# Kernel tuning notes

Hardware: AMD Instinct MI355X
Metric: run time of the kernel (lower is better)

The kernel has to match this reference:

```python
import jax, jax.numpy as jnp
import numpy as np
import math

NUM_HEADS = 16
HEAD_DIM = 64
ROPE_BASE = 10000.0

def _rope_tables(T, dtype):
    # inv_freq: (D/2,), emb = cat([freqs, freqs]) -> (T, D)
    inv_freq = 1.0 / (ROPE_BASE ** (jnp.arange(0, HEAD_DIM, 2, dtype=jnp.float32) / HEAD_DIM))
    t = jnp.arange(T, dtype=jnp.float32)
    freqs = jnp.einsum('i,j->ij', t, inv_freq)          # (T, D/2)
    emb = jnp.concatenate([freqs, freqs], axis=-1)      # (T, D)
    return jnp.cos(emb).astype(dtype), jnp.sin(emb).astype(dtype)

def _rotate_half(x):
    # interleaved pair rotation: (x0,x1,x2,x3,...) -> (-x1,x0,-x3,x2,...)
    x1 = x[..., ::2]
    x2 = x[..., 1::2]
    return jnp.stack((-x2, x1), axis=-1).reshape(x.shape)

def setup_inputs() -> dict:
    key = jax.random.key(0)
    ks = jax.random.split(key, 9)
    B, T, C = 2, 2048, 1024
    s = 1.0 / math.sqrt(C)
    return {
        'x':  jax.random.normal(ks[0], (B, T, C), dtype=jnp.float32),
        'wq': jax.random.normal(ks[1], (C, C), dtype=jnp.float32) * s,
        'bq': jax.random.normal(ks[2], (C,), dtype=jnp.float32) * s,
        'wk': jax.random.normal(ks[3], (C, C), dtype=jnp.float32) * s,
        'bk': jax.random.normal(ks[4], (C,), dtype=jnp.float32) * s,
        'wv': jax.random.normal(ks[5], (C, C), dtype=jnp.float32) * s,
        'bv': jax.random.normal(ks[6], (C,), dtype=jnp.float32) * s,
        'wo': jax.random.normal(ks[7], (C, C), dtype=jnp.float32) * s,
        'bo': jax.random.normal(ks[8], (C,), dtype=jnp.float32) * s,
    }

def reference(x, wq, bq, wk, bk, wv, bv, wo, bo):
    B, T, C = x.shape
    H, D = NUM_HEADS, HEAD_DIM

    def heads(t):  # (B,T,C) -> (B,H,T,D)
        return t.reshape(B, T, H, D).transpose(0, 2, 1, 3)

    q = heads(x @ wq.T + bq)
    k = heads(x @ wk.T + bk)
    v = heads(x @ wv.T + bv)

    cos, sin = _rope_tables(T, x.dtype)                 # (T, D)
    cos = cos[None, None]                               # (1,1,T,D)
    sin = sin[None, None]
    q = q * cos + _rotate_half(q) * sin
    k = k * cos + _rotate_half(k) * sin

    scores = jnp.einsum('bhqd,bhkd->bhqk', q, k) / math.sqrt(D)
    attn = jax.nn.softmax(scores, axis=-1)
    out = jnp.einsum('bhqk,bhkd->bhqd', attn, v)        # (B,H,T,D)
    out = out.transpose(0, 2, 1, 3).reshape(B, T, C)
    return out @ wo.T + bo
```

## Files before the change

### kernel.cpp

```cpp
#include <hip/hip_runtime.h>
#include <cmath>

#define TSEQ 2048
#define CDIM 1024
#define NHEAD 16
#define HDIM 64

typedef _Float16 half8 __attribute__((ext_vector_type(8)));
typedef _Float16 half4 __attribute__((ext_vector_type(4)));
typedef __fp16 fp16x2 __attribute__((ext_vector_type(2)));
typedef float f32x4 __attribute__((ext_vector_type(4)));
typedef float f32x16 __attribute__((ext_vector_type(16)));
typedef unsigned int u32x4 __attribute__((ext_vector_type(4)));

#define QSCALE   0.18033688011112042f
#define SHIFT_L2 12.984255368000671f

__device__ __forceinline__ void gload16(const void* g, void* l) {
    __builtin_amdgcn_global_load_lds((const __attribute__((address_space(1))) void*)g,
                                     (__attribute__((address_space(3))) void*)l, 16, 0, 0);
}

__device__ __forceinline__ unsigned int cvtpk_u32(float a, float b) {
    fp16x2 r = __builtin_amdgcn_cvt_pkrtz(a, b);
    return __builtin_bit_cast(unsigned int, r);
}

__global__ __launch_bounds__(256) void cvt_kernel(
    const float* __restrict__ x, const float* __restrict__ wq, const float* __restrict__ wk,
    const float* __restrict__ wv, const float* __restrict__ wo, _Float16* __restrict__ dst)
{
    const int y = blockIdx.y;
    const float* src;
    size_t cnt, doff;
    if (y == 0) { src = x; cnt = 4194304; doff = 0; }
    else {
        cnt = 1048576; doff = 4194304 + (size_t)(y - 1) * 1048576;
        src = (y == 1) ? wq : (y == 2) ? wk : (y == 3) ? wv : wo;
    }
    size_t i = ((size_t)blockIdx.x * 256 + threadIdx.x) * 4;
    if (i >= cnt) return;
    const float4 v = *(const float4*)(src + i);
    half4 h;
    h[0] = (_Float16)v.x; h[1] = (_Float16)v.y; h[2] = (_Float16)v.z; h[3] = (_Float16)v.w;
    *(half4*)(dst + doff + i) = h;
}

__global__ __launch_bounds__(256) void qkv_mfma_kernel(
    const _Float16* __restrict__ xh,
    const _Float16* __restrict__ wqh, const _Float16* __restrict__ wkh, const _Float16* __restrict__ wvh,
    const float* __restrict__ bq, const float* __restrict__ bk, const float* __restrict__ bv,
    _Float16* __restrict__ Qh, _Float16* __restrict__ Kh, _Float16* __restrict__ Vth)
{
    __shared__ __align__(16) _Float16 As[2 * 64 * 64];
    __shared__ __align__(16) _Float16 Bs[2 * 128 * 64];
    const int tid = threadIdx.x;
    const int lane = tid & 63, wid = tid >> 6;
    const int z = blockIdx.z;
    const _Float16* wh = (z == 0) ? wqh : (z == 1) ? wkh : wvh;
    const int m0 = blockIdx.y << 6, n0 = blockIdx.x << 7;

    const int srow = tid >> 3;
    const int sch = ((tid & 7) ^ (srow & 7)) * 8;
    const _Float16* gA = xh + (size_t)(m0 + srow) * CDIM + sch;
    const _Float16* gB = wh + (size_t)(n0 + srow) * CDIM + sch;
    _Float16* lA = As + tid * 8;
    _Float16* lB = Bs + tid * 8;

    const int cq = lane & 15, kg = lane >> 4;
    const int cx = cq & 7;

    f32x4 acc[4][2] = {};

    gload16(gA, lA);                 gload16(gA + (size_t)32 * CDIM, lA + 2048);
    gload16(gB, lB);                 gload16(gB + (size_t)32 * CDIM, lB + 2048);
    gload16(gB + (size_t)64 * CDIM, lB + 4096);
    gload16(gB + (size_t)96 * CDIM, lB + 6144);
    __syncthreads();

    for (int k0 = 0; k0 < CDIM; k0 += 64) {
        const int buf = (k0 >> 6) & 1;
        if (k0 + 64 < CDIM) {
            const int na = (buf ^ 1) * 4096, nb = (buf ^ 1) * 8192;
            gload16(gA + k0 + 64, lA + na);
            gload16(gA + (size_t)32 * CDIM + k0 + 64, lA + na + 2048);
            gload16(gB + k0 + 64, lB + nb);
            gload16(gB + (size_t)32 * CDIM + k0 + 64, lB + nb + 2048);
            gload16(gB + (size_t)64 * CDIM + k0 + 64, lB + nb + 4096);
            gload16(gB + (size_t)96 * CDIM + k0 + 64, lB + nb + 6144);
        }
        const _Float16* Ab = As + buf * 4096;
        const _Float16* Bb = Bs + buf * 8192;

        half8 af[4][2], bf[2][2];
#pragma unroll
        for (int i = 0; i < 4; ++i)
#pragma unroll
            for (int ks = 0; ks < 2; ++ks)
                af[i][ks] = *(const half8*)(Ab + (i * 16 + cq) * 64 + (((4 * ks + kg)) ^ cx) * 8);
#pragma unroll
        for (int j = 0; j < 2; ++j)
#pragma unroll
            for (int ks = 0; ks < 2; ++ks)
                bf[j][ks] = *(const half8*)(Bb + (wid * 32 + j * 16 + cq) * 64 + (((4 * ks + kg)) ^ cx) * 8);

        __builtin_amdgcn_s_setprio(1);
#pragma unroll
        for (int ks = 0; ks < 2; ++ks)
#pragma unroll
            for (int i = 0; i < 4; ++i)
#pragma unroll
                for (int j = 0; j < 2; ++j)
                    acc[i][j] = __builtin_amdgcn_mfma_f32_16x16x32_f16(af[i][ks], bf[j][ks], acc[i][j], 0, 0, 0);
        __builtin_amdgcn_s_setprio(0);
        __syncthreads();
    }

    if (z < 2) {
        const float* bias = z ? bk : bq;
        _Float16* dst = z ? Kh : Qh;
        const float qs = z ? 1.f : QSCALE;
#pragma unroll
        for (int fn = 0; fn < 2; ++fn) {
            int n = n0 + wid * 32 + fn * 16 + cq;
            int d = n & 63, h = n >> 6;
            float bs = bias[n];
            float fr = exp2f((float)(d & 31) * -0.41524101186092029f);
            float sgn = (d & 1) ? 1.f : -1.f;
#pragma unroll
            for (int fm = 0; fm < 4; ++fm) {
#pragma unroll
                for (int r = 0; r < 4; ++r) {
                    int m = m0 + fm * 16 + (kg << 2) + r;
                    int t = m & (TSEQ - 1), b = m >> 11;
                    float v = acc[fm][fn][r] + bs;
                    float prt = __shfl_xor(v, 1);
                    float sn, cs;
                    __sincosf((float)t * fr, &sn, &cs);
                    dst[(((size_t)(b * NHEAD + h)) * TSEQ + t) * HDIM + d] =
                        (_Float16)((v * cs + sgn * prt * sn) * qs);
                }
            }
        }
    } else {
#pragma unroll
        for (int fn = 0; fn < 2; ++fn) {
            int n = n0 + wid * 32 + fn * 16 + cq;
            int d = n & 63, h = n >> 6;
            float bs = bv[n];
#pragma unroll
            for (int fm = 0; fm < 4; ++fm) {
                int m = m0 + fm * 16 + (kg << 2);
                int t = m & (TSEQ - 1), b = m >> 11;
                half4 ov;
#pragma unroll
                for (int r = 0; r < 4; ++r) ov[r] = (_Float16)(acc[fm][fn][r] + bs);
                *(half4*)&Vth[(((size_t)(b * NHEAD + h)) * HDIM + d) * TSEQ + t] = ov;
            }
        }
    }
}

__global__ __launch_bounds__(256) void attn_mfma_kernel(
    const _Float16* __restrict__ Qh, const _Float16* __restrict__ Kh,
    const _Float16* __restrict__ Vth, _Float16* __restrict__ Ah)
{
    __shared__ __align__(16) _Float16 Ks[2 * 64 * 64];
    __shared__ __align__(16) _Float16 Vts[2 * 64 * 64];

    const int tid = threadIdx.x, lane = tid & 63, wid = tid >> 6;
    const int bh = blockIdx.y, q0 = blockIdx.x << 7;
    const size_t hb = (size_t)bh * TSEQ * HDIM;

    const int ql = lane & 31;
    const int hi = lane >> 5;
    const int lx = lane & 7;

    const int qrow = q0 + wid * 32 + ql;
    const _Float16* gq = Qh + hb + (size_t)qrow * HDIM + hi * 8;
    half8 bQ[4];
#pragma unroll
    for (int ks = 0; ks < 4; ++ks) bQ[ks] = *(const half8*)(gq + ks * 16);

    const int srow = tid >> 3;
    const int sch = ((tid & 7) ^ (srow & 7)) * 8;
    const _Float16* gK = Kh + hb + (size_t)srow * HDIM + sch;
    const _Float16* gV = Vth + hb + (size_t)srow * TSEQ + sch;
    _Float16* lK = Ks + tid * 8;
    _Float16* lV = Vts + tid * 8;

    f32x16 o0 = {}, o1 = {};
    float l_run = 0.f;
    f32x16 sinit;
#pragma unroll
    for (int i = 0; i < 16; ++i) sinit[i] = -SHIFT_L2;

    gload16(gK, lK);
    gload16(gK + 32 * HDIM, lK + 2048);
    gload16(gV, lV);
    gload16(gV + 32 * TSEQ, lV + 2048);
    __syncthreads();

    for (int kt = 0; kt < TSEQ / 64; ++kt) {
        const int buf = kt & 1;
        if (kt + 1 < TSEQ / 64) {
            const int nb = (buf ^ 1) * 4096;
            gload16(gK + (size_t)(kt + 1) * 64 * HDIM, lK + nb);
            gload16(gK + (size_t)(kt + 1) * 64 * HDIM + 32 * HDIM, lK + nb + 2048);
            gload16(gV + (kt + 1) * 64, lV + nb);
            gload16(gV + (kt + 1) * 64 + 32 * TSEQ, lV + nb + 2048);
        }
        const _Float16* Kb = Ks + buf * 4096;
        const _Float16* Vb = Vts + buf * 4096;

        f32x16 s0 = sinit, s1 = sinit;
        __builtin_amdgcn_s_setprio(1);
#pragma unroll
        for (int ks = 0; ks < 4; ++ks) {
            half8 k0 = *(const half8*)(Kb + ql * 64 + ((2 * ks + hi) ^ lx) * 8);
            half8 k1 = *(const half8*)(Kb + (32 + ql) * 64 + ((2 * ks + hi) ^ lx) * 8);
            s0 = __builtin_amdgcn_mfma_f32_32x32x16_f16(k0, bQ[ks], s0, 0, 0, 0);
            s1 = __builtin_amdgcn_mfma_f32_32x32x16_f16(k1, bQ[ks], s1, 0, 0, 0);
        }
        __builtin_amdgcn_s_setprio(0);

        f32x16 p0, p1;
#pragma unroll
        for (int i = 0; i < 16; ++i) p0[i] = __builtin_amdgcn_exp2f(s0[i]);
#pragma unroll
        for (int i = 0; i < 16; ++i) p1[i] = __builtin_amdgcn_exp2f(s1[i]);
        float ls = 0.f;
#pragma unroll
        for (int i = 0; i < 16; ++i) ls += p0[i] + p1[i];
        l_run += ls;

        half8 bP[4];
#pragma unroll
        for (int g = 0; g < 2; ++g) {
            const f32x16& p = g ? p1 : p0;
            unsigned int a0 = cvtpk_u32(p[0], p[1]),   a1 = cvtpk_u32(p[2], p[3]);
            unsigned int b0 = cvtpk_u32(p[4], p[5]),   b1 = cvtpk_u32(p[6], p[7]);
            unsigned int c0 = cvtpk_u32(p[8], p[9]),   c1 = cvtpk_u32(p[10], p[11]);
            unsigned int d0 = cvtpk_u32(p[12], p[13]), d1 = cvtpk_u32(p[14], p[15]);
            unsigned int sA = hi ? a0 : b0, sB = hi ? a1 : b1;
            unsigned int rA = __shfl_xor(sA, 32), rB = __shfl_xor(sB, 32);
            u32x4 w0 = { hi ? rA : a0, hi ? rB : a1, hi ? b0 : rA, hi ? b1 : rB };
            unsigned int sC = hi ? c0 : d0, sD = hi ? c1 : d1;
            unsigned int rC = __shfl_xor(sC, 32), rD = __shfl_xor(sD, 32);
            u32x4 w1 = { hi ? rC : c0, hi ? rD : c1, hi ? d0 : rC, hi ? d1 : rD };
            bP[2 * g]     = __builtin_bit_cast(half8, w0);
            bP[2 * g + 1] = __builtin_bit_cast(half8, w1);
        }

        __builtin_amdgcn_s_setprio(1);
#pragma unroll
        for (int ks = 0; ks < 4; ++ks) {
            half8 v0 = *(const half8*)(Vb + ql * 64 + ((2 * ks + hi) ^ lx) * 8);
            half8 v1 = *(const half8*)(Vb + (32 + ql) * 64 + ((2 * ks + hi) ^ lx) * 8);
            o0 = __builtin_amdgcn_mfma_f32_32x32x16_f16(v0, bP[ks], o0, 0, 0, 0);
            o1 = __builtin_amdgcn_mfma_f32_32x32x16_f16(v1, bP[ks], o1, 0, 0, 0);
        }
        __builtin_amdgcn_s_setprio(0);
        __syncthreads();
    }

    const int b = bh >> 4, hh = bh & 15;
    const float l_tot = l_run + __shfl_xor(l_run, 32);
    const float inv = 1.f / l_tot;
    const size_t rowoff = ((size_t)b * TSEQ + qrow) * CDIM + hh * 64;
#pragma unroll
    for (int dg = 0; dg < 2; ++dg) {
        const f32x16& o = dg ? o1 : o0;
#pragma unroll
        for (int j = 0; j < 4; ++j) {
            half4 ov;
#pragma unroll
            for (int c = 0; c < 4; ++c) ov[c] = (_Float16)(o[4 * j + c] * inv);
            *(half4*)&Ah[rowoff + dg * 32 + j * 8 + hi * 4] = ov;
        }
    }
}

__global__ __launch_bounds__(256) void oproj_mfma_kernel(
    const _Float16* __restrict__ Ahh, const _Float16* __restrict__ woh,
    const float* __restrict__ bo, float* __restrict__ out)
{
    __shared__ __align__(16) _Float16 As[2 * 64 * 64];
    __shared__ __align__(16) _Float16 Bs[2 * 128 * 64];
    const int tid = threadIdx.x;
    const int lane = tid & 63, wid = tid >> 6;
    const int m0 = blockIdx.y << 6, n0 = blockIdx.x << 7;

    const int srow = tid >> 3;
    const int sch = ((tid & 7) ^ (srow & 7)) * 8;
    const _Float16* gA = Ahh + (size_t)(m0 + srow) * CDIM + sch;
    const _Float16* gB = woh + (size_t)(n0 + srow) * CDIM + sch;
    _Float16* lA = As + tid * 8;
    _Float16* lB = Bs + tid * 8;

    const int cq = lane & 15, kg = lane >> 4;
    const int cx = cq & 7;

    f32x4 acc[4][2] = {};

    gload16(gA, lA);                 gload16(gA + (size_t)32 * CDIM, lA + 2048);
    gload16(gB, lB);                 gload16(gB + (size_t)32 * CDIM, lB + 2048);
    gload16(gB + (size_t)64 * CDIM, lB + 4096);
    gload16(gB + (size_t)96 * CDIM, lB + 6144);
    __syncthreads();

    for (int k0 = 0; k0 < CDIM; k0 += 64) {
        const int buf = (k0 >> 6) & 1;
        if (k0 + 64 < CDIM) {
            const int na = (buf ^ 1) * 4096, nb = (buf ^ 1) * 8192;
            gload16(gA + k0 + 64, lA + na);
            gload16(gA + (size_t)32 * CDIM + k0 + 64, lA + na + 2048);
            gload16(gB + k0 + 64, lB + nb);
            gload16(gB + (size_t)32 * CDIM + k0 + 64, lB + nb + 2048);
            gload16(gB + (size_t)64 * CDIM + k0 + 64, lB + nb + 4096);
            gload16(gB + (size_t)96 * CDIM + k0 + 64, lB + nb + 6144);
        }
        const _Float16* Ab = As + buf * 4096;
        const _Float16* Bb = Bs + buf * 8192;

        half8 af[4][2], bf[2][2];
#pragma unroll
        for (int i = 0; i < 4; ++i)
#pragma unroll
            for (int ks = 0; ks < 2; ++ks)
                af[i][ks] = *(const half8*)(Ab + (i * 16 + cq) * 64 + (((4 * ks + kg)) ^ cx) * 8);
#pragma unroll
        for (int j = 0; j < 2; ++j)
#pragma unroll
            for (int ks = 0; ks < 2; ++ks)
                bf[j][ks] = *(const half8*)(Bb + (wid * 32 + j * 16 + cq) * 64 + (((4 * ks + kg)) ^ cx) * 8);

        __builtin_amdgcn_s_setprio(1);
#pragma unroll
        for (int ks = 0; ks < 2; ++ks)
#pragma unroll
            for (int i = 0; i < 4; ++i)
#pragma unroll
                for (int j = 0; j < 2; ++j)
                    acc[i][j] = __builtin_amdgcn_mfma_f32_16x16x32_f16(af[i][ks], bf[j][ks], acc[i][j], 0, 0, 0);
        __builtin_amdgcn_s_setprio(0);
        __syncthreads();
    }

#pragma unroll
    for (int fn = 0; fn < 2; ++fn) {
        int n = n0 + wid * 32 + fn * 16 + cq;
        float bs = bo[n];
#pragma unroll
        for (int fm = 0; fm < 4; ++fm) {
#pragma unroll
            for (int r = 0; r < 4; ++r) {
                int m = m0 + fm * 16 + (kg << 2) + r;
                out[(size_t)m * CDIM + n] = acc[fm][fn][r] + bs;
            }
        }
    }
}

extern "C" void kernel_launch(void* const* d_in, const int* in_sizes, int n_in,
                              void* d_out, int out_size, void* d_ws, size_t ws_size,
                              hipStream_t stream) {
    (void)in_sizes; (void)n_in; (void)out_size; (void)ws_size;
    const float* x  = (const float*)d_in[0];
    const float* wq = (const float*)d_in[1];
    const float* bq = (const float*)d_in[2];
    const float* wk = (const float*)d_in[3];
    const float* bk = (const float*)d_in[4];
    const float* wv = (const float*)d_in[5];
    const float* bv = (const float*)d_in[6];
    const float* wo = (const float*)d_in[7];
    const float* bo = (const float*)d_in[8];
    float* out = (float*)d_out;

    _Float16* xh  = (_Float16*)d_ws;
    _Float16* wqh = xh + 4194304;
    _Float16* wkh = wqh + 1048576;
    _Float16* wvh = wkh + 1048576;
    _Float16* woh = wvh + 1048576;
    _Float16* Qh  = woh + 1048576;
    _Float16* Kh  = Qh + 4194304;
    _Float16* Vth = Kh + 4194304;
    _Float16* Ah  = Vth + 4194304;

    cvt_kernel<<<dim3(4096, 5), 256, 0, stream>>>(x, wq, wk, wv, wo, xh);
    qkv_mfma_kernel<<<dim3(8, 64, 3), 256, 0, stream>>>(xh, wqh, wkh, wvh, bq, bk, bv, Qh, Kh, Vth);
    attn_mfma_kernel<<<dim3(16, 32), 256, 0, stream>>>(Qh, Kh, Vth, Ah);
    oproj_mfma_kernel<<<dim3(8, 64), 256, 0, stream>>>(Ah, woh, bo, out);
}
```

Measured before the change: 128.1 us.

## Split attention key range across warps with LDS reduction and direct V loads

The attention kernel now processes 64 query rows per block and splits the key sequence into two halves handled by separate warp pairs. Their partial outputs and row sums are combined through shared memory at the end, and the grid doubles with a remapped block-to-head order. V is read straight from global memory into registers instead of being staged through LDS, and launch bounds request 4 blocks per CU. The goal is more parallelism and occupancy, but it adds a final reduction and relies on uncoalesced, unshared global V loads.

New measurement: 232.7 us. 81.6% more time.

```diff
diff --git a/kernel.cpp b/kernel.cpp
--- a/kernel.cpp
+++ b/kernel.cpp
@@ -161,33 +161,37 @@
     }
 }
 
-__global__ __launch_bounds__(256) void attn_mfma_kernel(
+__global__ __launch_bounds__(256, 4) void attn_mfma_kernel(
     const _Float16* __restrict__ Qh, const _Float16* __restrict__ Kh,
     const _Float16* __restrict__ Vth, _Float16* __restrict__ Ah)
 {
-    __shared__ __align__(16) _Float16 Ks[2 * 64 * 64];
-    __shared__ __align__(16) _Float16 Vts[2 * 64 * 64];
+    __shared__ __align__(16) _Float16 Ks[2 * 2 * 64 * 64];
 
     const int tid = threadIdx.x, lane = tid & 63, wid = tid >> 6;
-    const int bh = blockIdx.y, q0 = blockIdx.x << 7;
+    const int lin = blockIdx.x + 32 * blockIdx.y;
+    const int bh = (lin & 7) * 4 + ((lin >> 3) & 3);
+    const int q0 = (lin >> 5) << 6;
     const size_t hb = (size_t)bh * TSEQ * HDIM;
 
     const int ql = lane & 31;
     const int hi = lane >> 5;
     const int lx = lane & 7;
-
-    const int qrow = q0 + wid * 32 + ql;
+    const int qt = wid & 1;
+    const int kh = wid >> 1;
+    const int koff = kh << 10;
+
+    const int qrow = q0 + qt * 32 + ql;
     const _Float16* gq = Qh + hb + (size_t)qrow * HDIM + hi * 8;
     half8 bQ[4];
 #pragma unroll
     for (int ks = 0; ks < 4; ++ks) bQ[ks] = *(const half8*)(gq + ks * 16);
 
-    const int srow = tid >> 3;
-    const int sch = ((tid & 7) ^ (srow & 7)) * 8;
-    const _Float16* gK = Kh + hb + (size_t)srow * HDIM + sch;
-    const _Float16* gV = Vth + hb + (size_t)srow * TSEQ + sch;
-    _Float16* lK = Ks + tid * 8;
-    _Float16* lV = Vts + tid * 8;
+    const int portion = qt;
+    const _Float16* gKs = Kh + hb + (size_t)(koff + portion * 32 + (lane >> 3)) * HDIM
+                          + ((lane & 7) ^ ((lane >> 3) & 7)) * 8;
+    _Float16* lKs = Ks + kh * 8192 + portion * 2048 + lane * 8;
+
+    const _Float16* gVt = Vth + hb + koff;
 
     f32x16 o0 = {}, o1 = {};
     float l_run = 0.f;
@@ -195,23 +199,19 @@
 #pragma unroll
     for (int i = 0; i < 16; ++i) sinit[i] = -SHIFT_L2;
 
-    gload16(gK, lK);
-    gload16(gK + 32 * HDIM, lK + 2048);
-    gload16(gV, lV);
-    gload16(gV + 32 * TSEQ, lV + 2048);
+    gload16(gKs, lKs);           gload16(gKs + 512, lKs + 512);
+    gload16(gKs + 1024, lKs + 1024); gload16(gKs + 1536, lKs + 1536);
     __syncthreads();
 
-    for (int kt = 0; kt < TSEQ / 64; ++kt) {
+    for (int kt = 0; kt < 16; ++kt) {
         const int buf = kt & 1;
-        if (kt + 1 < TSEQ / 64) {
-            const int nb = (buf ^ 1) * 4096;
-            gload16(gK + (size_t)(kt + 1) * 64 * HDIM, lK + nb);
-            gload16(gK + (size_t)(kt + 1) * 64 * HDIM + 32 * HDIM, lK + nb + 2048);
-            gload16(gV + (kt + 1) * 64, lV + nb);
-            gload16(gV + (kt + 1) * 64 + 32 * TSEQ, lV + nb + 2048);
-        }
-        const _Float16* Kb = Ks + buf * 4096;
-        const _Float16* Vb = Vts + buf * 4096;
+        if (kt + 1 < 16) {
+            const _Float16* g = gKs + (size_t)(kt + 1) * 4096;
+            _Float16* l = lKs + (buf ^ 1) * 4096;
+            gload16(g, l);           gload16(g + 512, l + 512);
+            gload16(g + 1024, l + 1024); gload16(g + 1536, l + 1536);
+        }
+        const _Float16* Kb = Ks + kh * 8192 + buf * 4096;
 
         f32x16 s0 = sinit, s1 = sinit;
         __builtin_amdgcn_s_setprio(1);
@@ -223,6 +223,14 @@
             s1 = __builtin_amdgcn_mfma_f32_32x32x16_f16(k1, bQ[ks], s1, 0, 0, 0);
         }
         __builtin_amdgcn_s_setprio(0);
+
+        half8 vA[2][4];
+#pragma unroll
+        for (int dg = 0; dg < 2; ++dg)
+#pragma unroll
+            for (int ks = 0; ks < 4; ++ks)
+                vA[dg][ks] = *(const half8*)(gVt + (size_t)(dg * 32 + ql) * TSEQ
+                                             + kt * 64 + (2 * ks + hi) * 8);
 
         f32x16 p0, p1;
 #pragma unroll
@@ -255,28 +263,47 @@
         __builtin_amdgcn_s_setprio(1);
 #pragma unroll
         for (int ks = 0; ks < 4; ++ks) {
-            half8 v0 = *(const half8*)(Vb + ql * 64 + ((2 * ks + hi) ^ lx) * 8);
-            half8 v1 = *(const half8*)(Vb + (32 + ql) * 64 + ((2 * ks + hi) ^ lx) * 8);
-            o0 = __builtin_amdgcn_mfma_f32_32x32x16_f16(v0, bP[ks], o0, 0, 0, 0);
-            o1 = __builtin_amdgcn_mfma_f32_32x32x16_f16(v1, bP[ks], o1, 0, 0, 0);
+            o0 = __builtin_amdgcn_mfma_f32_32x32x16_f16(vA[0][ks], bP[ks], o0, 0, 0, 0);
+            o1 = __builtin_amdgcn_mfma_f32_32x32x16_f16(vA[1][ks], bP[ks], o1, 0, 0, 0);
         }
         __builtin_amdgcn_s_setprio(0);
         __syncthreads();
     }
 
-    const int b = bh >> 4, hh = bh & 15;
-    const float l_tot = l_run + __shfl_xor(l_run, 32);
-    const float inv = 1.f / l_tot;
-    const size_t rowoff = ((size_t)b * TSEQ + qrow) * CDIM + hh * 64;
-#pragma unroll
-    for (int dg = 0; dg < 2; ++dg) {
-        const f32x16& o = dg ? o1 : o0;
-#pragma unroll
-        for (int j = 0; j < 4; ++j) {
-            half4 ov;
-#pragma unroll
-            for (int c = 0; c < 4; ++c) ov[c] = (_Float16)(o[4 * j + c] * inv);
-            *(half4*)&Ah[rowoff + dg * 32 + j * 8 + hi * 4] = ov;
+    const float l_half = l_run + __shfl_xor(l_run, 32);
+    float* Ored = (float*)Ks;
+    float* Lsum = (float*)Ks + 4096;
+
+    if (wid >= 2) {
+#pragma unroll
+        for (int dg = 0; dg < 2; ++dg) {
+            const f32x16& o = dg ? o1 : o0;
+#pragma unroll
+            for (int r = 0; r < 16; ++r) {
+                int d = dg * 32 + (r & 3) + 8 * (r >> 2) + 4 * hi;
+                Ored[qt * 2048 + d * 32 + ql] = o[r];
+            }
+        }
+        if (!hi) Lsum[qt * 32 + ql] = l_half;
+    }
+    __syncthreads();
+    if (wid < 2) {
+        const int b = bh >> 4, hh = bh & 15;
+        const float inv = 1.f / (l_half + Lsum[qt * 32 + ql]);
+        const size_t rowoff = ((size_t)b * TSEQ + qrow) * CDIM + hh * 64;
+#pragma unroll
+        for (int dg = 0; dg < 2; ++dg) {
+            const f32x16& o = dg ? o1 : o0;
+#pragma unroll
+            for (int j = 0; j < 4; ++j) {
+                half4 ov;
+#pragma unroll
+                for (int c = 0; c < 4; ++c) {
+                    int d = dg * 32 + 8 * j + 4 * hi + c;
+                    ov[c] = (_Float16)((o[4 * j + c] + Ored[qt * 2048 + d * 32 + ql]) * inv);
+                }
+                *(half4*)&Ah[rowoff + dg * 32 + j * 8 + hi * 4] = ov;
+            }
         }
     }
 }
@@ -389,6 +416,6 @@
 
     cvt_kernel<<<dim3(4096, 5), 256, 0, stream>>>(x, wq, wk, wv, wo, xh);
     qkv_mfma_kernel<<<dim3(8, 64, 3), 256, 0, stream>>>(xh, wqh, wkh, wvh, bq, bk, bv, Qh, Kh, Vth);
-    attn_mfma_kernel<<<dim3(16, 32), 256, 0, stream>>>(Qh, Kh, Vth, Ah);
+    attn_mfma_kernel<<<dim3(32, 32), 256, 0, stream>>>(Qh, Kh, Vth, Ah);
     oproj_mfma_kernel<<<dim3(8, 64), 256, 0, stream>>>(Ah, woh, bo, out);
 }
```
